# Kernel optimization log

Measured on AMD Instinct MI355X. Metric: run time of the kernel, lower is better.

## Reference

```python
import jax, jax.numpy as jnp
import numpy as np
from functools import partial

EPS = 1e-6

def rmsnorm(x, w):
    rms = jnp.sqrt(jnp.mean(x * x, axis=-1, keepdims=True) + EPS)
    return x * w / rms

def causal_dwconv(x, w):
    # x: [B, T, D], w: [D, 1, k] depthwise kernel (torch Conv1d layout)
    D = x.shape[-1]
    k = w.shape[-1]
    xt = jnp.transpose(x, (0, 2, 1))  # [B, D, T]
    out = jax.lax.conv_general_dilated(
        xt, w, window_strides=(1,), padding=[(k - 1, 0)],
        dimension_numbers=("NCH", "OIH", "NCH"), feature_group_count=D)
    return jnp.transpose(out, (0, 2, 1))  # [B, T, D]

def setup_inputs() -> dict:
    key = jax.random.key(0)
    B, T, D, F, S = 2, 4096, 1024, 4096, 4096
    ks = jax.random.split(key, 20)
    s = 0.02
    return {
        "x": jax.random.normal(ks[0], (B, T, D), jnp.float32),
        "h_prev": jnp.zeros((B, D), jnp.float32),
        "norm1_w": jnp.ones((D,), jnp.float32),
        "conv3_w": jax.random.normal(ks[1], (D, 1, 3), jnp.float32) * s,
        "conv7_w": jax.random.normal(ks[2], (D, 1, 7), jnp.float32) * s,
        "conv15_w": jax.random.normal(ks[3], (D, 1, 15), jnp.float32) * s,
        "mix_w": jax.random.normal(ks[4], (D, D), jnp.float32) * s,
        "norm2_w": jnp.ones((D,), jnp.float32),
        "Wz_w": jax.random.normal(ks[5], (D, D), jnp.float32) * s,
        "Wz_b": jnp.zeros((D,), jnp.float32),
        "Wh_w": jax.random.normal(ks[6], (D, D), jnp.float32) * s,
        "Wh_b": jnp.zeros((D,), jnp.float32),
        "norm3_w": jnp.ones((D,), jnp.float32),
        "slot_keys": jax.random.normal(ks[7], (S, D), jnp.float32) * s,
        "slot_values": jax.random.normal(ks[8], (S, D), jnp.float32) * s,
        "projq_w": jax.random.normal(ks[9], (D, D), jnp.float32) * s,
        "projout_w": jax.random.normal(ks[10], (D, D), jnp.float32) * s,
        "norm4_w": jnp.ones((D,), jnp.float32),
        "gate_w": jax.random.normal(ks[11], (F, D), jnp.float32) * s,
        "up_w": jax.random.normal(ks[12], (F, D), jnp.float32) * s,
        "down_w": jax.random.normal(ks[13], (D, F), jnp.float32) * s,
    }

def resonance_forward(x, h_prev, norm1_w, conv3_w, conv7_w, conv15_w, mix_w,
                      norm2_w, Wz_w, Wz_b, Wh_w, Wh_b, norm3_w, slot_keys,
                      slot_values, projq_w, projout_w, norm4_w, gate_w, up_w, down_w):
    B, T, D = x.shape
    top_k = 2
    # 1. multi-scale causal conv block
    xn = rmsnorm(x, norm1_w)
    conv = causal_dwconv(xn, conv3_w) + causal_dwconv(xn, conv7_w) + causal_dwconv(xn, conv15_w)
    x = x + conv @ mix_w.T
    # 2. MinGRU: precompute gates, then linear recurrence via scan
    xn = rmsnorm(x, norm2_w)
    z = jax.nn.sigmoid(xn @ Wz_w.T + Wz_b)        # [B, T, D]
    h_tilde = xn @ Wh_w.T + Wh_b                  # [B, T, D]
    def step(h, zh):
        zt, ht = zh
        h = (1.0 - zt) * h + zt * ht
        return h, h
    h_last, hs = jax.lax.scan(step, h_prev,
                              (jnp.swapaxes(z, 0, 1), jnp.swapaxes(h_tilde, 0, 1)))
    x = x + jnp.swapaxes(hs, 0, 1)
    # 3. slot memory with top-k routing
    xn = rmsnorm(x, norm3_w)
    q = xn @ projq_w.T
    scores = (q @ slot_keys.T) / jnp.sqrt(jnp.asarray(D, x.dtype))  # [B, T, S]
    topk_vals, topk_ids = jax.lax.top_k(scores, top_k)              # [B, T, k]
    attn = jax.nn.softmax(topk_vals, axis=-1)
    gathered = slot_values[topk_ids]                                # [B, T, k, D]
    retrieved = jnp.einsum("btk,btkd->btd", attn, gathered)
    x = x + retrieved @ projout_w.T
    # 4. SwiGLU FFN
    xn = rmsnorm(x, norm4_w)
    ff = (jax.nn.silu(xn @ gate_w.T) * (xn @ up_w.T)) @ down_w.T
    x = x + ff
    return x, h_last

def reference(x, h_prev, norm1_w, conv3_w, conv7_w, conv15_w, mix_w, norm2_w,
              Wz_w, Wz_b, Wh_w, Wh_b, norm3_w, slot_keys, slot_values,
              projq_w, projout_w, norm4_w, gate_w, up_w, down_w):
    return resonance_forward(x, h_prev, norm1_w, conv3_w, conv7_w, conv15_w,
                             mix_w, norm2_w, Wz_w, Wz_b, Wh_w, Wh_b, norm3_w,
                             slot_keys, slot_values, projq_w, projout_w,
                             norm4_w, gate_w, up_w, down_w)
```

## Files before the change

kernel.cpp:

```cpp
#include <hip/hip_runtime.h>
#include <hip/hip_bf16.h>
#include <cstdint>
#include <cfloat>
#include <climits>

#define BB   2
#define TT   4096
#define DD   1024
#define FF   4096
#define SS   4096
#define MTOK (BB * TT)
#define NCHUNK 32
#define TCHUNK 128

typedef __bf16 bf16x8 __attribute__((ext_vector_type(8)));
typedef float  f32x4  __attribute__((ext_vector_type(4)));
typedef __attribute__((address_space(3))) char lds_char;
typedef __attribute__((address_space(1))) char g_char;

#define TKMERGE(w0, j0, w1, j1)                                              \
  {                                                                          \
    if (w0 > v0 || (w0 == v0 && j0 < i0)) {                                  \
      float t0v = v0; int t0i = i0; v0 = w0; i0 = j0;                        \
      if (t0v > w1 || (t0v == w1 && t0i < j1)) { v1 = t0v; i1 = t0i; }       \
      else { v1 = w1; i1 = j1; }                                             \
    } else {                                                                 \
      if (w0 > v1 || (w0 == v1 && j0 < i1)) { v1 = w0; i1 = j0; }            \
    }                                                                        \
  }

struct CvtArgs {
  const float* src[10];
  __hip_bfloat16* dst[10];
  int off4[11];
  int mode[10];
};

__global__ __launch_bounds__(256) void cvt_all_kernel(CvtArgs a) {
  int g = blockIdx.x * 256 + threadIdx.x;
  if (g >= a.off4[10]) return;
  int s = 0;
  while (g >= a.off4[s + 1]) s++;
  int i = g - a.off4[s];
  float4 v = ((const float4*)a.src[s])[i];
  union { ushort4 u; __hip_bfloat16 h[4]; } p;
  p.h[0] = __float2bfloat16(v.x);
  p.h[1] = __float2bfloat16(v.y);
  p.h[2] = __float2bfloat16(v.z);
  p.h[3] = __float2bfloat16(v.w);
  int m = a.mode[s];
  if (m == 3) {
    int r = i >> 8, c4 = i & 255;
#pragma unroll
    for (int k = 0; k < 4; k++)
      a.dst[s][(size_t)(c4 * 4 + k) * 1024 + r] = p.h[k];
    return;
  }
  int di = i;
  if (m == 1 || m == 2) {
    int r = i >> 8, c = i & 255;
    int dr = ((r >> 4) << 5) + (r & 15) + ((m == 2) ? 16 : 0);
    di = (dr << 8) + c;
  }
  ((ushort4*)a.dst[s])[di] = p.u;
}

__global__ void wcomb_kernel(const float* __restrict__ w3, const float* __restrict__ w7,
                             const float* __restrict__ w15, float* __restrict__ wc) {
  int d = blockIdx.x * 256 + threadIdx.x;
  if (d >= DD) return;
  for (int j = 0; j < 16; j++) {
    float v = 0.f;
    if (j < 15) {
      v = w15[d * 15 + (14 - j)];
      if (j < 7) v += w7[d * 7 + (6 - j)];
      if (j < 3) v += w3[d * 3 + (2 - j)];
    }
    wc[d * 16 + j] = v;
  }
}

template <int INBF16>
__global__ __launch_bounds__(256) void rms_kernel(const void* __restrict__ xv,
                                                  const float* __restrict__ w,
                                                  __hip_bfloat16* __restrict__ ob) {
  const int row = blockIdx.x;
  const int tid = threadIdx.x;
  float4 v;
  if constexpr (INBF16) {
    union { ushort4 u; __hip_bfloat16 h[4]; } q;
    q.u = ((const ushort4*)((const __hip_bfloat16*)xv + (size_t)row * DD))[tid];
    v.x = __bfloat162float(q.h[0]); v.y = __bfloat162float(q.h[1]);
    v.z = __bfloat162float(q.h[2]); v.w = __bfloat162float(q.h[3]);
  } else {
    v = ((const float4*)((const float*)xv + (size_t)row * DD))[tid];
  }
  float ss = v.x * v.x + v.y * v.y + v.z * v.z + v.w * v.w;
  for (int off = 32; off > 0; off >>= 1) ss += __shfl_down(ss, off, 64);
  __shared__ float wsum[4];
  if ((tid & 63) == 0) wsum[tid >> 6] = ss;
  __syncthreads();
  float tot = wsum[0] + wsum[1] + wsum[2] + wsum[3];
  float rinv = 1.0f / sqrtf(tot * (1.0f / DD) + 1e-6f);
  float4 wg = ((const float4*)w)[tid];
  union { ushort4 u; __hip_bfloat16 h[4]; } p;
  p.h[0] = __float2bfloat16(v.x * wg.x * rinv);
  p.h[1] = __float2bfloat16(v.y * wg.y * rinv);
  p.h[2] = __float2bfloat16(v.z * wg.z * rinv);
  p.h[3] = __float2bfloat16(v.w * wg.w * rinv);
  ((ushort4*)ob)[(size_t)row * 256 + tid] = p.u;
}

__global__ __launch_bounds__(256) void conv_kernel(const __hip_bfloat16* __restrict__ xn,
                                                   const float* __restrict__ wc,
                                                   __hip_bfloat16* __restrict__ outp) {
  __shared__ float xt[78][64];
  __shared__ float wt[64][15];
  const int b = blockIdx.z, t0 = blockIdx.x * 64, d0 = blockIdx.y * 64;
  const int tid = threadIdx.x;
  const int dl = tid & 63;
  for (int idx = tid; idx < 64 * 15; idx += 256) {
    int d = idx / 15, j = idx % 15;
    wt[d][j] = wc[(d0 + d) * 16 + j];
  }
  for (int r = tid >> 6; r < 78; r += 4) {
    int t = t0 - 14 + r;
    xt[r][dl] = (t >= 0) ? __bfloat162float(xn[((size_t)b * TT + t) * DD + d0 + dl]) : 0.f;
  }
  __syncthreads();
  for (int tl = tid >> 6; tl < 64; tl += 4) {
    float acc = 0.f;
#pragma unroll
    for (int j = 0; j < 15; j++) acc += wt[dl][j] * xt[tl + 14 - j][dl];
    outp[((size_t)b * TT + t0 + tl) * DD + d0 + dl] = __float2bfloat16(acc);
  }
}

template <int EPI, int KSPLIT = 1, int SWZ = 0>
__global__ __launch_bounds__(256, 2) void gemm_bt(
    const __hip_bfloat16* __restrict__ A, const __hip_bfloat16* __restrict__ Bm,
    const int M, const int N, const int K,
    float* __restrict__ outf, __hip_bfloat16* __restrict__ outb,
    const float* __restrict__ bias0, const float* __restrict__ bias1) {
  __shared__ __align__(16) __hip_bfloat16 As[2][128 * 32];
  __shared__ __align__(16) __hip_bfloat16 Bs[2][128 * 32];
  const int tid = threadIdx.x;
  const int lane = tid & 63;
  const int wave = tid >> 6;
  const int fm = lane & 15, fq = lane >> 4;

  const int nT = gridDim.x;
  const int lin = blockIdx.y * nT + blockIdx.x;
  int tileM, tileN;
  if constexpr (SWZ == 0) {
    const int xcd = lin & 7;
    const int idx_ = lin >> 3;
    const int mq = idx_ / nT;
    tileM = (xcd * (gridDim.y >> 3) + mq) * 128;
    tileN = (idx_ - mq * nT) * 128;
  } else {
    const int xcd = lin & 7;
    const int idx_ = lin >> 3;
    const int nS = nT >> 3;
    const int m = idx_ / nS;
    const int nl = idx_ - m * nS;
    tileM = m * 128;
    tileN = (xcd * nS + nl) * 128;
  }

  const int wm = (wave & 1) * 64, wn = (wave >> 1) * 64;

  f32x4 acc[4][4] = {};

  const int srow = tid >> 2;
  const int scol = (tid & 3) * 8;
  const __hip_bfloat16* gA = A + (size_t)(tileM + srow) * K + scol;
  const __hip_bfloat16* gB = Bm + (size_t)(tileN + srow) * K + scol;
  lds_char* ldsA0 = (lds_char*)(&As[0][0]);
  lds_char* ldsA1 = (lds_char*)(&As[1][0]);
  lds_char* ldsB0 = (lds_char*)(&Bs[0][0]);
  lds_char* ldsB1 = (lds_char*)(&Bs[1][0]);
  const int wbyte = wave * 1024;

  const int kPer = K / KSPLIT;
  const int kBeg = (KSPLIT > 1) ? blockIdx.z * kPer : 0;
  for (int k0 = kBeg; k0 < kBeg + kPer; k0 += 64) {
    __syncthreads();
    __builtin_amdgcn_global_load_lds((g_char*)(void*)(gA + k0),                       ldsA0 + wbyte,        16, 0, 0);
    __builtin_amdgcn_global_load_lds((g_char*)(void*)(gA + k0 + (size_t)64 * K),      ldsA0 + wbyte + 4096, 16, 0, 0);
    __builtin_amdgcn_global_load_lds((g_char*)(void*)(gB + k0),                       ldsB0 + wbyte,        16, 0, 0);
    __builtin_amdgcn_global_load_lds((g_char*)(void*)(gB + k0 + (size_t)64 * K),      ldsB0 + wbyte + 4096, 16, 0, 0);
    __builtin_amdgcn_global_load_lds((g_char*)(void*)(gA + k0 + 32),                  ldsA1 + wbyte,        16, 0, 0);
    __builtin_amdgcn_global_load_lds((g_char*)(void*)(gA + k0 + 32 + (size_t)64 * K), ldsA1 + wbyte + 4096, 16, 0, 0);
    __builtin_amdgcn_global_load_lds((g_char*)(void*)(gB + k0 + 32),                  ldsB1 + wbyte,        16, 0, 0);
    __builtin_amdgcn_global_load_lds((g_char*)(void*)(gB + k0 + 32 + (size_t)64 * K), ldsB1 + wbyte + 4096, 16, 0, 0);
    __syncthreads();
#pragma unroll
    for (int s = 0; s < 2; s++) {
      bf16x8 af[4], bfr[4];
#pragma unroll
      for (int i = 0; i < 4; i++) {
        af[i]  = *(const bf16x8*)(&As[s][0] + (wm + i * 16 + fm) * 32 + fq * 8);
        bfr[i] = *(const bf16x8*)(&Bs[s][0] + (wn + i * 16 + fm) * 32 + fq * 8);
      }
#pragma unroll
      for (int i = 0; i < 4; i++)
#pragma unroll
        for (int j = 0; j < 4; j++)
          acc[i][j] = __builtin_amdgcn_mfma_f32_16x16x32_bf16(af[i], bfr[j], acc[i][j], 0, 0, 0);
    }
  }

  if constexpr (EPI == 7) {
#pragma unroll
    for (int i = 0; i < 4; i++) {
#pragma unroll
      for (int j = 0; j < 4; j += 2) {
        const int ffcol = (((tileN + wn + j * 16) >> 5) << 4) + fm;
#pragma unroll
        for (int r = 0; r < 4; r++) {
          const int rw = tileM + wm + i * 16 + fq * 4 + r;
          float g = acc[i][j][r];
          float u = acc[i][j + 1][r];
          float v = g / (1.f + __expf(-g)) * u;
          outb[(size_t)rw * FF + ffcol] = __float2bfloat16(v);
        }
      }
    }
  } else if constexpr (EPI == 8) {
    __shared__ float lv2[2][128][2];
    __shared__ int   li2[2][128][2];
    const int half = wn >> 6;
#pragma unroll
    for (int i = 0; i < 4; i++) {
#pragma unroll
      for (int r = 0; r < 4; r++) {
        float v0 = -FLT_MAX, v1 = -FLT_MAX;
        int i0 = INT_MAX, i1 = INT_MAX;
#pragma unroll
        for (int j = 0; j < 4; j++) {
          float v = acc[i][j][r];
          int c = tileN + wn + j * 16 + fm;
          if (v > v0) { v1 = v0; i1 = i0; v0 = v; i0 = c; }
          else if (v > v1) { v1 = v; i1 = c; }
        }
#pragma unroll
        for (int off = 1; off < 16; off <<= 1) {
          float w0 = __shfl_xor(v0, off, 64), w1 = __shfl_xor(v1, off, 64);
          int   j0 = __shfl_xor(i0, off, 64), j1 = __shfl_xor(i1, off, 64);
          TKMERGE(w0, j0, w1, j1);
        }
        if (fm == 0) {
          const int lrow = wm + i * 16 + fq * 4 + r;
          lv2[half][lrow][0] = v0; lv2[half][lrow][1] = v1;
          li2[half][lrow][0] = i0; li2[half][lrow][1] = i1;
        }
      }
    }
    __syncthreads();
    if (tid < 128) {
      float v0 = lv2[0][tid][0], v1 = lv2[0][tid][1];
      int   i0 = li2[0][tid][0], i1 = li2[0][tid][1];
      float w0 = lv2[1][tid][0], w1 = lv2[1][tid][1];
      int   j0 = li2[1][tid][0], j1 = li2[1][tid][1];
      TKMERGE(w0, j0, w1, j1);
      float4 c4;
      c4.x = v0; c4.y = v1;
      c4.z = __int_as_float(i0); c4.w = __int_as_float(i1);
      ((float4*)outf)[(size_t)(tileM + tid) * (SS / 128) + (tileN >> 7)] = c4;
    }
  } else {
#pragma unroll
    for (int i = 0; i < 4; i++) {
#pragma unroll
      for (int j = 0; j < 4; j++) {
        const int c = tileN + wn + j * 16 + fm;
#pragma unroll
        for (int r = 0; r < 4; r++) {
          const int rw = tileM + wm + i * 16 + fq * 4 + r;
          const size_t idx = (size_t)rw * N + c;
          float v = acc[i][j][r];
          if constexpr (EPI == 1) {
            v += (c < DD) ? bias0[c] : bias1[c - DD];
            if (c < DD) v = 1.f / (1.f + __expf(-v));
            outb[idx] = __float2bfloat16(v);
          } else if constexpr (EPI == 2) {
            outb[idx] = __float2bfloat16(v);
          } else if constexpr (EPI == 6) {
            outb[(size_t)blockIdx.z * M * N + idx] = __float2bfloat16(v);
          }
        }
      }
    }
  }
}

template <int EPI>
__global__ __launch_bounds__(256, 4) void gemm_bt64(
    const __hip_bfloat16* __restrict__ A, const __hip_bfloat16* __restrict__ Bm,
    const int M, const int N, const int K,
    const float* __restrict__ residf, const __hip_bfloat16* __restrict__ residb,
    __hip_bfloat16* __restrict__ outb) {
  __shared__ __align__(16) __hip_bfloat16 As[2][64 * 32];
  __shared__ __align__(16) __hip_bfloat16 Bs[2][128 * 32];
  const int tid = threadIdx.x;
  const int lane = tid & 63;
  const int wave = tid >> 6;
  const int fm = lane & 15, fq = lane >> 4;

  const int nT = gridDim.x;
  const int lin = blockIdx.y * nT + blockIdx.x;
  const int xcd = lin & 7;
  const int idx_ = lin >> 3;
  const int mq = idx_ / nT;
  const int tileM = (xcd * (gridDim.y >> 3) + mq) * 64;
  const int tileN = (idx_ - mq * nT) * 128;

  const int wm = (wave & 1) * 32, wn = (wave >> 1) * 64;

  f32x4 acc[2][4] = {};

  const int srow = tid >> 2;
  const int scol = (tid & 3) * 8;
  const __hip_bfloat16* gA = A + (size_t)(tileM + srow) * K + scol;
  const __hip_bfloat16* gB = Bm + (size_t)(tileN + srow) * K + scol;
  lds_char* ldsA0 = (lds_char*)(&As[0][0]);
  lds_char* ldsA1 = (lds_char*)(&As[1][0]);
  lds_char* ldsB0 = (lds_char*)(&Bs[0][0]);
  lds_char* ldsB1 = (lds_char*)(&Bs[1][0]);
  const int wbyte = wave * 1024;

  for (int k0 = 0; k0 < K; k0 += 64) {
    __syncthreads();
    __builtin_amdgcn_global_load_lds((g_char*)(void*)(gA + k0),                       ldsA0 + wbyte,        16, 0, 0);
    __builtin_amdgcn_global_load_lds((g_char*)(void*)(gB + k0),                       ldsB0 + wbyte,        16, 0, 0);
    __builtin_amdgcn_global_load_lds((g_char*)(void*)(gB + k0 + (size_t)64 * K),      ldsB0 + wbyte + 4096, 16, 0, 0);
    __builtin_amdgcn_global_load_lds((g_char*)(void*)(gA + k0 + 32),                  ldsA1 + wbyte,        16, 0, 0);
    __builtin_amdgcn_global_load_lds((g_char*)(void*)(gB + k0 + 32),                  ldsB1 + wbyte,        16, 0, 0);
    __builtin_amdgcn_global_load_lds((g_char*)(void*)(gB + k0 + 32 + (size_t)64 * K), ldsB1 + wbyte + 4096, 16, 0, 0);
    __syncthreads();
#pragma unroll
    for (int s = 0; s < 2; s++) {
      bf16x8 af[2], bfr[4];
#pragma unroll
      for (int i = 0; i < 2; i++)
        af[i]  = *(const bf16x8*)(&As[s][0] + (wm + i * 16 + fm) * 32 + fq * 8);
#pragma unroll
      for (int j = 0; j < 4; j++)
        bfr[j] = *(const bf16x8*)(&Bs[s][0] + (wn + j * 16 + fm) * 32 + fq * 8);
#pragma unroll
      for (int i = 0; i < 2; i++)
#pragma unroll
        for (int j = 0; j < 4; j++)
          acc[i][j] = __builtin_amdgcn_mfma_f32_16x16x32_bf16(af[i], bfr[j], acc[i][j], 0, 0, 0);
    }
  }

#pragma unroll
  for (int i = 0; i < 2; i++) {
#pragma unroll
    for (int j = 0; j < 4; j++) {
      const int c = tileN + wn + j * 16 + fm;
#pragma unroll
      for (int r = 0; r < 4; r++) {
        const int rw = tileM + wm + i * 16 + fq * 4 + r;
        const size_t idx = (size_t)rw * N + c;
        float v = acc[i][j][r];
        if constexpr (EPI == 0) {
          outb[idx] = __float2bfloat16(residf[idx] + v);
        } else {
          outb[idx] = __float2bfloat16(__bfloat162float(residb[idx]) + v);
        }
      }
    }
  }
}

__global__ __launch_bounds__(256) void reduce_final(const __hip_bfloat16* __restrict__ P,
                                                    const __hip_bfloat16* __restrict__ resid,
                                                    float* __restrict__ out) {
  size_t i = (size_t)blockIdx.x * 256 + threadIdx.x;
  bf16x8 a = ((const bf16x8*)P)[i];
  bf16x8 b = ((const bf16x8*)(P + (size_t)MTOK * DD))[i];
  bf16x8 rr = ((const bf16x8*)resid)[i];
  float o[8];
#pragma unroll
  for (int k = 0; k < 8; k++)
    o[k] = (float)rr[k] + (float)a[k] + (float)b[k];
  float4 o0 = {o[0], o[1], o[2], o[3]};
  float4 o1 = {o[4], o[5], o[6], o[7]};
  ((float4*)out)[i * 2]     = o0;
  ((float4*)out)[i * 2 + 1] = o1;
}

__global__ __launch_bounds__(256) void scan_pass1(const __hip_bfloat16* __restrict__ zht,
                                                  float* __restrict__ cA,
                                                  float* __restrict__ cB) {
  const int b = blockIdx.z, c = blockIdx.y;
  const int d = blockIdx.x * 256 + threadIdx.x;
  const __hip_bfloat16* base = zht + (size_t)b * TT * 2048;
  float A = 1.f, Bc = 0.f;
  const int t0 = c * TCHUNK;
  for (int t = t0; t < t0 + TCHUNK; t++) {
    const __hip_bfloat16* rowp = base + (size_t)t * 2048;
    float z = __bfloat162float(rowp[d]);
    float h = __bfloat162float(rowp[DD + d]);
    float om = 1.f - z;
    A *= om;
    Bc = om * Bc + z * h;
  }
  size_t idx = ((size_t)b * NCHUNK + c) * DD + d;
  cA[idx] = A;
  cB[idx] = Bc;
}

__global__ __launch_bounds__(256) void scan_pass2(const float* __restrict__ hp,
                                                  const float* __restrict__ cA,
                                                  const float* __restrict__ cB,
                                                  float* __restrict__ hstart,
                                                  float* __restrict__ hlast) {
  const int b = blockIdx.y;
  const int d = blockIdx.x * 256 + threadIdx.x;
  float h = hp[b * DD + d];
  for (int c = 0; c < NCHUNK; c++) {
    size_t idx = ((size_t)b * NCHUNK + c) * DD + d;
    hstart[idx] = h;
    h = cA[idx] * h + cB[idx];
  }
  hlast[b * DD + d] = h;
}

__global__ __launch_bounds__(256) void scan_pass3(const __hip_bfloat16* __restrict__ zht,
                                                  const float* __restrict__ hstart,
                                                  __hip_bfloat16* __restrict__ x) {
  const int b = blockIdx.z, c = blockIdx.y;
  const int d = blockIdx.x * 256 + threadIdx.x;
  const __hip_bfloat16* base = zht + (size_t)b * TT * 2048;
  float h = hstart[((size_t)b * NCHUNK + c) * DD + d];
  const int t0 = c * TCHUNK;
  for (int t = t0; t < t0 + TCHUNK; t++) {
    const __hip_bfloat16* rowp = base + (size_t)t * 2048;
    float z = __bfloat162float(rowp[d]);
    float ht = __bfloat162float(rowp[DD + d]);
    h = (1.f - z) * h + z * ht;
    size_t xi = ((size_t)b * TT + t) * DD + d;
    x[xi] = __float2bfloat16(__bfloat162float(x[xi]) + h);
  }
}

__global__ __launch_bounds__(256) void topk_merge(const float4* __restrict__ cand,
                                                  const __hip_bfloat16* __restrict__ svb,
                                                  __hip_bfloat16* __restrict__ ret) {
  const int row = blockIdx.x * 4 + (threadIdx.x >> 6);
  const int lane = threadIdx.x & 63;
  float v0 = -FLT_MAX, v1 = -FLT_MAX;
  int i0 = INT_MAX, i1 = INT_MAX;
  if (lane < 32) {
    float4 c = cand[(size_t)row * 32 + lane];
    v0 = c.x; v1 = c.y;
    i0 = __float_as_int(c.z); i1 = __float_as_int(c.w);
  }
#pragma unroll
  for (int off = 1; off < 64; off <<= 1) {
    float w0 = __shfl_xor(v0, off, 64), w1 = __shfl_xor(v1, off, 64);
    int   j0 = __shfl_xor(i0, off, 64), j1 = __shfl_xor(i1, off, 64);
    TKMERGE(w0, j0, w1, j1);
  }
  float s0 = v0 * (1.f / 32.f), s1 = v1 * (1.f / 32.f);
  float e = __expf(s1 - s0);
  float denom = 1.f + e;
  float a0 = 1.f / denom;
  float a1 = e / denom;
  const bf16x8* r0 = (const bf16x8*)(svb + (size_t)i0 * DD);
  const bf16x8* r1 = (const bf16x8*)(svb + (size_t)i1 * DD);
#pragma unroll
  for (int k = 0; k < 2; k++) {
    int j = lane + 64 * k;
    bf16x8 u = r0[j], w8 = r1[j];
    bf16x8 res;
#pragma unroll
    for (int t = 0; t < 8; t++)
      res[t] = (__bf16)(a0 * (float)u[t] + a1 * (float)w8[t]);
    ((bf16x8*)(ret + (size_t)row * DD))[j] = res;
  }
}

extern "C" void kernel_launch(void* const* d_in, const int* in_sizes, int n_in,
                              void* d_out, int out_size, void* d_ws, size_t ws_size,
                              hipStream_t stream) {
  (void)in_sizes; (void)n_in; (void)out_size; (void)ws_size;
  const float* x_in   = (const float*)d_in[0];
  const float* h_prev = (const float*)d_in[1];
  const float* n1w    = (const float*)d_in[2];
  const float* w3     = (const float*)d_in[3];
  const float* w7     = (const float*)d_in[4];
  const float* w15    = (const float*)d_in[5];
  const float* mixw   = (const float*)d_in[6];
  const float* n2w    = (const float*)d_in[7];
  const float* wzw    = (const float*)d_in[8];
  const float* wzb    = (const float*)d_in[9];
  const float* whw    = (const float*)d_in[10];
  const float* whb    = (const float*)d_in[11];
  const float* n3w    = (const float*)d_in[12];
  const float* slotk  = (const float*)d_in[13];
  const float* slotv  = (const float*)d_in[14];
  const float* pqw    = (const float*)d_in[15];
  const float* pow_   = (const float*)d_in[16];
  const float* n4w    = (const float*)d_in[17];
  const float* gatew  = (const float*)d_in[18];
  const float* upw    = (const float*)d_in[19];
  const float* downw  = (const float*)d_in[20];
  float* out = (float*)d_out;

  char* ws = (char*)d_ws;
  size_t o = 0;
  auto alloc = [&](size_t bytes) {
    size_t r = o;
    o += (bytes + 255) & ~(size_t)255;
    return r;
  };
  __hip_bfloat16* wmix = (__hip_bfloat16*)(ws + alloc((size_t)DD * DD * 2));
  __hip_bfloat16* wzht = (__hip_bfloat16*)(ws + alloc((size_t)2 * DD * DD * 2));
  __hip_bfloat16* wpqT = (__hip_bfloat16*)(ws + alloc((size_t)DD * DD * 2));
  __hip_bfloat16* wsk  = (__hip_bfloat16*)(ws + alloc((size_t)SS * DD * 2));
  __hip_bfloat16* wpo  = (__hip_bfloat16*)(ws + alloc((size_t)DD * DD * 2));
  __hip_bfloat16* wfu  = (__hip_bfloat16*)(ws + alloc((size_t)2 * FF * DD * 2));
  __hip_bfloat16* wd   = (__hip_bfloat16*)(ws + alloc((size_t)DD * FF * 2));
  __hip_bfloat16* w2b  = (__hip_bfloat16*)(ws + alloc((size_t)SS * DD * 2));
  __hip_bfloat16* svb  = (__hip_bfloat16*)(ws + alloc((size_t)SS * DD * 2));
  float* wcomb = (float*)(ws + alloc((size_t)DD * 16 * 4));
  __hip_bfloat16* xws  = (__hip_bfloat16*)(ws + alloc((size_t)MTOK * DD * 2));
  __hip_bfloat16* xnb  = (__hip_bfloat16*)(ws + alloc((size_t)MTOK * DD * 2));
  __hip_bfloat16* retr = (__hip_bfloat16*)(ws + alloc((size_t)MTOK * DD * 2));
  float* scanA  = (float*)(ws + alloc((size_t)BB * NCHUNK * DD * 4));
  float* scanB  = (float*)(ws + alloc((size_t)BB * NCHUNK * DD * 4));
  float* hstart = (float*)(ws + alloc((size_t)BB * NCHUNK * DD * 4));
  char* big = ws + alloc((size_t)MTOK * FF * 4);
  __hip_bfloat16* xn1b  = (__hip_bfloat16*)big;
  __hip_bfloat16* convb = (__hip_bfloat16*)(big + (size_t)MTOK * DD * 2);
  __hip_bfloat16* zhtb  = (__hip_bfloat16*)big;
  float* candf          = (float*)big;
  __hip_bfloat16* ffin  = (__hip_bfloat16*)big;
  __hip_bfloat16* Pbuf  = (__hip_bfloat16*)(big + (size_t)MTOK * FF * 2);

  {
    CvtArgs a;
    const float* srcs[10] = {mixw, wzw, whw, pqw, slotk, pow_, gatew, upw, downw, slotv};
    __hip_bfloat16* dsts[10] = {wmix, wzht, wzht + (size_t)DD * DD, wpqT, wsk, wpo, wfu, wfu, wd, svb};
    int n4s[10] = {DD * DD / 4, DD * DD / 4, DD * DD / 4, DD * DD / 4, SS * DD / 4,
                   DD * DD / 4, FF * DD / 4, FF * DD / 4, DD * FF / 4, SS * DD / 4};
    int modes[10] = {0, 0, 0, 3, 0, 0, 1, 2, 0, 0};
    int acc_ = 0;
    for (int i = 0; i < 10; i++) {
      a.src[i] = srcs[i]; a.dst[i] = dsts[i]; a.off4[i] = acc_; a.mode[i] = modes[i];
      acc_ += n4s[i];
    }
    a.off4[10] = acc_;
    cvt_all_kernel<<<(acc_ + 255) / 256, 256, 0, stream>>>(a);
  }
  wcomb_kernel<<<DD / 256, 256, 0, stream>>>(w3, w7, w15, wcomb);
  gemm_bt<2, 1, 0><<<dim3(DD / 128, SS / 128), 256, 0, stream>>>(
      wsk, wpqT, SS, DD, DD, nullptr, w2b, nullptr, nullptr);

  rms_kernel<0><<<MTOK, 256, 0, stream>>>(x_in, n1w, xn1b);
  conv_kernel<<<dim3(TT / 64, DD / 64, BB), 256, 0, stream>>>(xn1b, wcomb, convb);
  gemm_bt64<0><<<dim3(DD / 128, MTOK / 64), 256, 0, stream>>>(
      convb, wmix, MTOK, DD, DD, x_in, nullptr, xws);

  rms_kernel<1><<<MTOK, 256, 0, stream>>>(xws, n2w, xnb);
  gemm_bt<1, 1, 0><<<dim3(2048 / 128, MTOK / 128), 256, 0, stream>>>(
      xnb, wzht, MTOK, 2048, DD, nullptr, zhtb, wzb, whb);
  scan_pass1<<<dim3(DD / 256, NCHUNK, BB), 256, 0, stream>>>(zhtb, scanA, scanB);
  scan_pass2<<<dim3(DD / 256, BB), 256, 0, stream>>>(h_prev, scanA, scanB, hstart,
                                                     out + (size_t)MTOK * DD);
  scan_pass3<<<dim3(DD / 256, NCHUNK, BB), 256, 0, stream>>>(zhtb, hstart, xws);

  rms_kernel<1><<<MTOK, 256, 0, stream>>>(xws, n3w, xnb);
  gemm_bt<8, 1, 1><<<dim3(SS / 128, MTOK / 128), 256, 0, stream>>>(
      xnb, w2b, MTOK, SS, DD, candf, nullptr, nullptr, nullptr);
  topk_merge<<<MTOK / 4, 256, 0, stream>>>((const float4*)candf, svb, retr);
  gemm_bt64<3><<<dim3(DD / 128, MTOK / 64), 256, 0, stream>>>(
      retr, wpo, MTOK, DD, DD, nullptr, xws, xws);

  rms_kernel<1><<<MTOK, 256, 0, stream>>>(xws, n4w, xnb);
  gemm_bt<7, 1, 1><<<dim3(2 * FF / 128, MTOK / 128), 256, 0, stream>>>(
      xnb, wfu, MTOK, 2 * FF, DD, nullptr, ffin, nullptr, nullptr);
  gemm_bt<6, 2, 0><<<dim3(DD / 128, MTOK / 128, 2), 256, 0, stream>>>(
      ffin, wd, MTOK, DD, FF, nullptr, Pbuf, nullptr, nullptr);
  reduce_final<<<MTOK * DD / 2048, 256, 0, stream>>>(Pbuf, xws, out);
}
```

Measured before the change: 741.9 us.

## Fuse scan chunk-summary pass into Wz/Wh GEMM epilogue with interleaved z/h layout

The Wz/Wh GEMM epilogue now computes the gated-scan chunk summaries (A, B) directly from the accumulators using shuffle-based combines across lanes and an LDS merge across waves, which eliminates the separate scan_pass1 kernel and its full re-read of the z/h buffer. The weight conversion interleaves Wz and Wh rows (modes 1/2) so each 32-column group holds paired z and h columns, and z/h are stored interleaved as bf16 pairs so scan_pass3 reads them with one 32-bit load. The slot-key precompute GEMM is also switched to the 64-row tile variant. The change adds epilogue complexity and depends on the chunk size matching the 128-row GEMM tile.

```diff
diff --git a/kernel.cpp b/kernel.cpp
--- a/kernel.cpp
+++ b/kernel.cpp
@@ -140,7 +140,8 @@
 __global__ __launch_bounds__(256, 2) void gemm_bt(
     const __hip_bfloat16* __restrict__ A, const __hip_bfloat16* __restrict__ Bm,
     const int M, const int N, const int K,
-    float* __restrict__ outf, __hip_bfloat16* __restrict__ outb,
+    float* __restrict__ outf, float* __restrict__ outf2,
+    __hip_bfloat16* __restrict__ outb,
     const float* __restrict__ bias0, const float* __restrict__ bias1) {
   __shared__ __align__(16) __hip_bfloat16 As[2][128 * 32];
   __shared__ __align__(16) __hip_bfloat16 Bs[2][128 * 32];
@@ -269,6 +270,61 @@
       c4.z = __int_as_float(i0); c4.w = __int_as_float(i1);
       ((float4*)outf)[(size_t)(tileM + tid) * (SS / 128) + (tileN >> 7)] = c4;
     }
+  } else if constexpr (EPI == 9) {
+    __shared__ float scA[2][64], scB[2][64];
+    const int half = wm >> 6;
+#pragma unroll
+    for (int jp = 0; jp < 2; jp++) {
+      const int c_even = tileN + wn + jp * 32 + fm;
+      const int d = ((c_even >> 5) << 4) + fm;
+      const float bz = bias0[d], bh = bias1[d];
+      float Afull = 1.f, Bfull = 0.f;
+#pragma unroll
+      for (int i = 0; i < 4; i++) {
+        float Ar = 1.f, Br = 0.f;
+#pragma unroll
+        for (int r = 0; r < 4; r++) {
+          float z  = 1.f / (1.f + __expf(-(acc[i][2 * jp][r] + bz)));
+          float ht = acc[i][2 * jp + 1][r] + bh;
+          const int t = tileM + wm + i * 16 + fq * 4 + r;
+          union { uint32_t u; __hip_bfloat16 h[2]; } pz;
+          pz.h[0] = __float2bfloat16(z);
+          pz.h[1] = __float2bfloat16(ht);
+          *(uint32_t*)(outb + (size_t)t * 2048 + 2 * d) = pz.u;
+          float a = 1.f - z;
+          Br = a * Br + z * ht;
+          Ar = a * Ar;
+        }
+        {
+          float Ao = __shfl_xor(Ar, 16, 64), Bo = __shfl_xor(Br, 16, 64);
+          if (fq & 1) { Br = Ar * Bo + Br; Ar = Ar * Ao; }
+          else        { Br = Ao * Br + Bo; Ar = Ao * Ar; }
+        }
+        {
+          float Ao = __shfl_xor(Ar, 32, 64), Bo = __shfl_xor(Br, 32, 64);
+          if (fq & 2) { Br = Ar * Bo + Br; Ar = Ar * Ao; }
+          else        { Br = Ao * Br + Bo; Ar = Ao * Ar; }
+        }
+        Bfull = Ar * Bfull + Br;
+        Afull = Ar * Afull;
+      }
+      if (fq == 0) {
+        const int dl = (((wn + jp * 32) >> 5) << 4) + fm;
+        scA[half][dl] = Afull;
+        scB[half][dl] = Bfull;
+      }
+    }
+    __syncthreads();
+    if (tid < 64) {
+      float A0 = scA[0][tid], B0 = scB[0][tid];
+      float A1 = scA[1][tid], B1 = scB[1][tid];
+      const int b = tileM >> 12;
+      const int c = (tileM & 4095) >> 7;
+      const int d = (tileN >> 1) + tid;
+      const size_t idx = ((size_t)b * NCHUNK + c) * DD + d;
+      outf[idx]  = A1 * A0;
+      outf2[idx] = A1 * B0 + B1;
+    }
   } else {
 #pragma unroll
     for (int i = 0; i < 4; i++) {
@@ -280,11 +336,7 @@
           const int rw = tileM + wm + i * 16 + fq * 4 + r;
           const size_t idx = (size_t)rw * N + c;
           float v = acc[i][j][r];
-          if constexpr (EPI == 1) {
-            v += (c < DD) ? bias0[c] : bias1[c - DD];
-            if (c < DD) v = 1.f / (1.f + __expf(-v));
-            outb[idx] = __float2bfloat16(v);
-          } else if constexpr (EPI == 2) {
+          if constexpr (EPI == 2) {
             outb[idx] = __float2bfloat16(v);
           } else if constexpr (EPI == 6) {
             outb[(size_t)blockIdx.z * M * N + idx] = __float2bfloat16(v);
@@ -368,6 +420,8 @@
         float v = acc[i][j][r];
         if constexpr (EPI == 0) {
           outb[idx] = __float2bfloat16(residf[idx] + v);
+        } else if constexpr (EPI == 2) {
+          outb[idx] = __float2bfloat16(v);
         } else {
           outb[idx] = __float2bfloat16(__bfloat162float(residb[idx]) + v);
         }
@@ -391,27 +445,6 @@
   float4 o1 = {o[4], o[5], o[6], o[7]};
   ((float4*)out)[i * 2]     = o0;
   ((float4*)out)[i * 2 + 1] = o1;
-}
-
-__global__ __launch_bounds__(256) void scan_pass1(const __hip_bfloat16* __restrict__ zht,
-                                                  float* __restrict__ cA,
-                                                  float* __restrict__ cB) {
-  const int b = blockIdx.z, c = blockIdx.y;
-  const int d = blockIdx.x * 256 + threadIdx.x;
-  const __hip_bfloat16* base = zht + (size_t)b * TT * 2048;
-  float A = 1.f, Bc = 0.f;
-  const int t0 = c * TCHUNK;
-  for (int t = t0; t < t0 + TCHUNK; t++) {
-    const __hip_bfloat16* rowp = base + (size_t)t * 2048;
-    float z = __bfloat162float(rowp[d]);
-    float h = __bfloat162float(rowp[DD + d]);
-    float om = 1.f - z;
-    A *= om;
-    Bc = om * Bc + z * h;
-  }
-  size_t idx = ((size_t)b * NCHUNK + c) * DD + d;
-  cA[idx] = A;
-  cB[idx] = Bc;
 }
 
 __global__ __launch_bounds__(256) void scan_pass2(const float* __restrict__ hp,
@@ -439,9 +472,10 @@
   float h = hstart[((size_t)b * NCHUNK + c) * DD + d];
   const int t0 = c * TCHUNK;
   for (int t = t0; t < t0 + TCHUNK; t++) {
-    const __hip_bfloat16* rowp = base + (size_t)t * 2048;
-    float z = __bfloat162float(rowp[d]);
-    float ht = __bfloat162float(rowp[DD + d]);
+    union { uint32_t u; __hip_bfloat16 hh[2]; } q;
+    q.u = *(const uint32_t*)(base + (size_t)t * 2048 + 2 * d);
+    float z  = __bfloat162float(q.hh[0]);
+    float ht = __bfloat162float(q.hh[1]);
     h = (1.f - z) * h + z * ht;
     size_t xi = ((size_t)b * TT + t) * DD + d;
     x[xi] = __float2bfloat16(__bfloat162float(x[xi]) + h);
@@ -546,10 +580,10 @@
   {
     CvtArgs a;
     const float* srcs[10] = {mixw, wzw, whw, pqw, slotk, pow_, gatew, upw, downw, slotv};
-    __hip_bfloat16* dsts[10] = {wmix, wzht, wzht + (size_t)DD * DD, wpqT, wsk, wpo, wfu, wfu, wd, svb};
+    __hip_bfloat16* dsts[10] = {wmix, wzht, wzht, wpqT, wsk, wpo, wfu, wfu, wd, svb};
     int n4s[10] = {DD * DD / 4, DD * DD / 4, DD * DD / 4, DD * DD / 4, SS * DD / 4,
                    DD * DD / 4, FF * DD / 4, FF * DD / 4, DD * FF / 4, SS * DD / 4};
-    int modes[10] = {0, 0, 0, 3, 0, 0, 1, 2, 0, 0};
+    int modes[10] = {0, 1, 2, 3, 0, 0, 1, 2, 0, 0};
     int acc_ = 0;
     for (int i = 0; i < 10; i++) {
       a.src[i] = srcs[i]; a.dst[i] = dsts[i]; a.off4[i] = acc_; a.mode[i] = modes[i];
@@ -559,8 +593,8 @@
     cvt_all_kernel<<<(acc_ + 255) / 256, 256, 0, stream>>>(a);
   }
   wcomb_kernel<<<DD / 256, 256, 0, stream>>>(w3, w7, w15, wcomb);
-  gemm_bt<2, 1, 0><<<dim3(DD / 128, SS / 128), 256, 0, stream>>>(
-      wsk, wpqT, SS, DD, DD, nullptr, w2b, nullptr, nullptr);
+  gemm_bt64<2><<<dim3(DD / 128, SS / 64), 256, 0, stream>>>(
+      wsk, wpqT, SS, DD, DD, nullptr, nullptr, w2b);
 
   rms_kernel<0><<<MTOK, 256, 0, stream>>>(x_in, n1w, xn1b);
   conv_kernel<<<dim3(TT / 64, DD / 64, BB), 256, 0, stream>>>(xn1b, wcomb, convb);
@@ -568,24 +602,23 @@
       convb, wmix, MTOK, DD, DD, x_in, nullptr, xws);
 
   rms_kernel<1><<<MTOK, 256, 0, stream>>>(xws, n2w, xnb);
-  gemm_bt<1, 1, 0><<<dim3(2048 / 128, MTOK / 128), 256, 0, stream>>>(
-      xnb, wzht, MTOK, 2048, DD, nullptr, zhtb, wzb, whb);
-  scan_pass1<<<dim3(DD / 256, NCHUNK, BB), 256, 0, stream>>>(zhtb, scanA, scanB);
+  gemm_bt<9, 1, 0><<<dim3(2048 / 128, MTOK / 128), 256, 0, stream>>>(
+      xnb, wzht, MTOK, 2048, DD, scanA, scanB, zhtb, wzb, whb);
   scan_pass2<<<dim3(DD / 256, BB), 256, 0, stream>>>(h_prev, scanA, scanB, hstart,
                                                      out + (size_t)MTOK * DD);
   scan_pass3<<<dim3(DD / 256, NCHUNK, BB), 256, 0, stream>>>(zhtb, hstart, xws);
 
   rms_kernel<1><<<MTOK, 256, 0, stream>>>(xws, n3w, xnb);
   gemm_bt<8, 1, 1><<<dim3(SS / 128, MTOK / 128), 256, 0, stream>>>(
-      xnb, w2b, MTOK, SS, DD, candf, nullptr, nullptr, nullptr);
+      xnb, w2b, MTOK, SS, DD, candf, nullptr, nullptr, nullptr, nullptr);
   topk_merge<<<MTOK / 4, 256, 0, stream>>>((const float4*)candf, svb, retr);
   gemm_bt64<3><<<dim3(DD / 128, MTOK / 64), 256, 0, stream>>>(
       retr, wpo, MTOK, DD, DD, nullptr, xws, xws);
 
   rms_kernel<1><<<MTOK, 256, 0, stream>>>(xws, n4w, xnb);
   gemm_bt<7, 1, 1><<<dim3(2 * FF / 128, MTOK / 128), 256, 0, stream>>>(
-      xnb, wfu, MTOK, 2 * FF, DD, nullptr, ffin, nullptr, nullptr);
+      xnb, wfu, MTOK, 2 * FF, DD, nullptr, nullptr, ffin, nullptr, nullptr);
   gemm_bt<6, 2, 0><<<dim3(DD / 128, MTOK / 128, 2), 256, 0, stream>>>(
-      ffin, wd, MTOK, DD, FF, nullptr, Pbuf, nullptr, nullptr);
+      ffin, wd, MTOK, DD, FF, nullptr, nullptr, Pbuf, nullptr, nullptr);
   reduce_final<<<MTOK * DD / 2048, 256, 0, stream>>>(Pbuf, xws, out);
 }
```

New measurement: 744.3 us. No clear change (+0.3%).
